# Kernel optimization log

Measured on AMD Instinct MI355X. Metric: run time of the kernel, lower is better.

The kernel has to match this reference:

```python
import jax, jax.numpy as jnp
import numpy as np

N_NODES = 100000
N_EDGES = 1600000
NEG_SLOPE = 0.2


def gat_layer(x, edge_index, W, att_src, att_dst, bias, concat):
    """PyG-style GATConv (v1) with self-loops added, dropout=0."""
    N = x.shape[0]
    H, C = att_src.shape
    ar = jnp.arange(N)
    src = jnp.concatenate([edge_index[0], ar])  # add self-loops
    dst = jnp.concatenate([edge_index[1], ar])
    h = (x @ W).reshape(N, H, C)                # [N,H,C]
    a_src = jnp.sum(h * att_src[None], axis=-1)  # [N,H]
    a_dst = jnp.sum(h * att_dst[None], axis=-1)  # [N,H]
    e = jax.nn.leaky_relu(a_src[src] + a_dst[dst], NEG_SLOPE)  # [E,H]
    # segment softmax over destination nodes
    m = jax.ops.segment_max(e, dst, num_segments=N)
    e = jnp.exp(e - m[dst])
    s = jax.ops.segment_sum(e, dst, num_segments=N)
    alpha = e / (s[dst] + 1e-16)                # [E,H]
    msg = h[src] * alpha[:, :, None]            # [E,H,C]
    out = jax.ops.segment_sum(msg, dst, num_segments=N)  # [N,H,C]
    if concat:
        out = out.reshape(N, H * C)
    else:
        out = out.mean(axis=1)
    return out + bias


def prelu(x, a):
    return jnp.where(x >= 0, x, a * x)


def setup_inputs() -> dict:
    key = jax.random.key(0)
    ks = jax.random.split(key, 12)
    def g(k, shape, fan):
        return jax.random.normal(k, shape, dtype=jnp.float32) * (1.0 / np.sqrt(fan))
    x = jax.random.normal(ks[0], (N_NODES, 256), dtype=jnp.float32)
    edge_index = jax.random.randint(ks[1], (2, N_EDGES), 0, N_NODES, dtype=jnp.int64 if jax.config.read('jax_enable_x64') else jnp.int32)
    return {
        'x': x,
        'edge_index': edge_index,
        'W1': g(ks[2], (256, 64), 256), 'as1': g(ks[3], (8, 8), 8), 'ad1': g(ks[4], (8, 8), 8), 'b1': jnp.zeros((64,), jnp.float32),
        'W2': g(ks[5], (320, 64), 320), 'as2': g(ks[6], (8, 8), 8), 'ad2': g(ks[7], (8, 8), 8), 'b2': jnp.zeros((64,), jnp.float32),
        'W3': g(ks[8], (64, 128), 64), 'as3': g(ks[9], (8, 16), 16), 'ad3': g(ks[10], (8, 16), 16), 'b3': jnp.zeros((16,), jnp.float32),
        'p1': jnp.full((1,), 0.25, jnp.float32), 'p2': jnp.full((1,), 0.25, jnp.float32),
    }


def reference(x, edge_index, W1, as1, ad1, b1, W2, as2, ad2, b2, W3, as3, ad3, b3, p1, p2):
    h = gat_layer(x, edge_index, W1, as1, ad1, b1, concat=True)
    h = prelu(h, p1)
    h = gat_layer(jnp.concatenate([x, h], axis=1), edge_index, W2, as2, ad2, b2, concat=True)
    h = prelu(h, p2)
    h = gat_layer(h, edge_index, W3, as3, ad3, b3, concat=False)
    return jax.nn.log_softmax(h, axis=1)
```

## Files before the change

kernel.cpp:

```cpp
#include <hip/hip_runtime.h>
#include <hip/hip_bf16.h>
#include <stdint.h>

typedef unsigned short u16;
typedef __attribute__((ext_vector_type(8))) short short8;
typedef __attribute__((ext_vector_type(8))) __bf16 bf16x8;
typedef __attribute__((ext_vector_type(4))) float f32x4;
typedef __attribute__((ext_vector_type(4))) float fv4;

#define DEV static __device__ __forceinline__

DEV float bf2f(u16 u) { uint32_t i = ((uint32_t)u) << 16; float f; __builtin_memcpy(&f, &i, 4); return f; }
DEV u16 f2bf(float f) {
    uint32_t i; __builtin_memcpy(&i, &f, 4);
    uint32_t r = i + 0x7FFFu + ((i >> 16) & 1u);
    return (u16)(r >> 16);
}
DEV float lo16f(uint32_t u) { uint32_t i = u << 16; float f; __builtin_memcpy(&f, &i, 4); return f; }
DEV float hi16f(uint32_t u) { uint32_t i = u & 0xFFFF0000u; float f; __builtin_memcpy(&f, &i, 4); return f; }
DEV uint32_t pack2(float a, float b) { return (uint32_t)f2bf(a) | ((uint32_t)f2bf(b) << 16); }
DEV float lrelu(float x) { return x >= 0.f ? x : 0.2f * x; }

#define CHK 4096
#define BN2SH 10
#define BN2 1024

__global__ __launch_bounds__(256) void k_cvt(const float* __restrict__ in, u16* __restrict__ out, int n4) {
    int i = blockIdx.x * 256 + threadIdx.x;
    if (i < n4) {
        fv4 v = __builtin_nontemporal_load((const fv4*)in + i);
        uint64_t o = (uint64_t)f2bf(v.x) | ((uint64_t)f2bf(v.y) << 16)
                   | ((uint64_t)f2bf(v.z) << 32) | ((uint64_t)f2bf(v.w) << 48);
        __builtin_nontemporal_store(o, (uint64_t*)out + i);
    }
}

__global__ __launch_bounds__(256) void k_hist(const int* __restrict__ dst, int* __restrict__ hist,
                                              int NBUK, int nbp, int E) {
    __shared__ int h[BN2];
    int tid = threadIdx.x;
    for (int i = tid; i < NBUK; i += 256) h[i] = 0;
    __syncthreads();
    int b0 = blockIdx.x * CHK;
    int jend = b0 + CHK < E ? b0 + CHK : E;
    for (int j = b0 + tid; j < jend; j += 256)
        atomicAdd(&h[dst[j] >> BN2SH], 1);
    __syncthreads();
    for (int i = tid; i < NBUK; i += 256) hist[i * nbp + blockIdx.x] = h[i];
}

__global__ void k_scanpart(const int* __restrict__ deg, int* __restrict__ bsum, int n) {
    __shared__ int buf[1024];
    int tid = threadIdx.x;
    int i = blockIdx.x * 1024 + tid;
    int v = (i < n) ? deg[i] : 0;
    buf[tid] = v; __syncthreads();
    for (int d = 512; d > 0; d >>= 1) {
        if (tid < d) buf[tid] += buf[tid + d];
        __syncthreads();
    }
    if (tid == 0) bsum[blockIdx.x] = buf[0];
}

__global__ void k_scanbsum(int* bsum, int nb) {
    if (threadIdx.x == 0) {
        int run = 0;
        for (int b = 0; b < nb; ++b) { int t = bsum[b]; bsum[b] = run; run += t; }
    }
}

__global__ void k_scanonly(const int* __restrict__ in, const int* __restrict__ bsum,
                           int* __restrict__ out, int n) {
    __shared__ int buf[1024];
    int tid = threadIdx.x;
    int i = blockIdx.x * 1024 + tid;
    int v = (i < n) ? in[i] : 0;
    buf[tid] = v; __syncthreads();
    for (int d = 1; d < 1024; d <<= 1) {
        int t = (tid >= d) ? buf[tid - d] : 0;
        __syncthreads();
        buf[tid] += t;
        __syncthreads();
    }
    if (i < n) out[i] = buf[tid] - v + bsum[blockIdx.x];
}

__global__ __launch_bounds__(256) void k_part(const int* __restrict__ src, const int* __restrict__ dst,
                                              const int* __restrict__ scanned, int* __restrict__ stage,
                                              int NBUK, int nbp, int E) {
    __shared__ int cur[BN2];
    int tid = threadIdx.x;
    for (int i = tid; i < NBUK; i += 256) cur[i] = scanned[i * nbp + blockIdx.x];
    __syncthreads();
    int b0 = blockIdx.x * CHK;
    int jend = b0 + CHK < E ? b0 + CHK : E;
    for (int j = b0 + tid; j < jend; j += 256) {
        int d = dst[j];
        int p = atomicAdd(&cur[d >> BN2SH], 1);
        stage[p] = src[j] | ((d & (BN2 - 1)) << 17);
    }
}

__global__ __launch_bounds__(256) void k_csr(const int* __restrict__ stage, const int* __restrict__ scanned,
                                             int* __restrict__ off, int* __restrict__ srt,
                                             int NBUK, int nbp, int N, int E) {
    __shared__ int deg[BN2];
    __shared__ int ex[BN2];
    __shared__ int tsum[256];
    int tid = threadIdx.x, b = blockIdx.x;
    int base = b << BN2SH;
    int s0 = scanned[b * nbp];
    int s1 = (b + 1 < NBUK) ? scanned[(b + 1) * nbp] : E;
    for (int i = tid; i < BN2; i += 256) deg[i] = 0;
    __syncthreads();
    for (int j = s0 + tid; j < s1; j += 256) atomicAdd(&deg[(uint32_t)stage[j] >> 17], 1);
    __syncthreads();
    int t4 = tid * 4;
    int d0 = deg[t4], d1 = deg[t4 + 1], d2 = deg[t4 + 2], d3 = deg[t4 + 3];
    int tot = d0 + d1 + d2 + d3;
    tsum[tid] = tot; __syncthreads();
    for (int d = 1; d < 256; d <<= 1) {
        int t = (tid >= d) ? tsum[tid - d] : 0;
        __syncthreads();
        tsum[tid] += t;
        __syncthreads();
    }
    int ebase = tsum[tid] - tot;
    ex[t4] = ebase; ex[t4 + 1] = ebase + d0; ex[t4 + 2] = ebase + d0 + d1; ex[t4 + 3] = ebase + d0 + d1 + d2;
    __syncthreads();
    for (int i = tid; i < BN2; i += 256) { int n = base + i; if (n < N) off[n] = s0 + ex[i]; }
    if (b == 0 && tid == 0) off[N] = E;
    __syncthreads();
    for (int j = s0 + tid; j < s1; j += 256) {
        int sd = stage[j];
        int p = atomicAdd(&ex[(uint32_t)sd >> 17], 1);
        srt[s0 + p] = sd & 0x1FFFF;
    }
}

__global__ __launch_bounds__(256) void gemm_k(const u16* __restrict__ A1, int K1,
                                              const u16* __restrict__ A2, int K2,
                                              const float* __restrict__ W, int M,
                                              u16* __restrict__ out, int N) {
    __shared__ u16 wt[64][328];
    __shared__ u16 As[64][40];
    const int K = K1 + K2;
    const int tid = threadIdx.x;
    const int n0 = blockIdx.x * 64;
    const int cb = blockIdx.y * 64;

    for (int idx = tid; idx < K * 64; idx += 256) {
        int k = idx >> 6, m = idx & 63;
        wt[m][k] = f2bf(W[(size_t)k * M + cb + m]);
    }

    const int wv = tid >> 6, lane = tid & 63;
    const int quad = lane >> 4, r = lane & 15;
    f32x4 acc[4];
#pragma unroll
    for (int ct = 0; ct < 4; ++ct) acc[ct] = (f32x4){0.f, 0.f, 0.f, 0.f};

    const int row = tid >> 2, seg = tid & 3;
    const int gl = n0 + row;

    for (int k0 = 0; k0 < K; k0 += 32) {
        int4 v = {0, 0, 0, 0};
        if (gl < N) {
            const u16* base = (k0 < K1) ? (A1 + (size_t)gl * K1 + k0)
                                        : (A2 + (size_t)gl * K2 + (k0 - K1));
            v = *(const int4*)(base + seg * 8);
        }
        *(int4*)&As[row][seg * 8] = v;
        __syncthreads();
        bf16x8 a = __builtin_bit_cast(bf16x8, *(const short8*)&As[wv * 16 + r][quad * 8]);
#pragma unroll
        for (int ct = 0; ct < 4; ++ct) {
            bf16x8 b = __builtin_bit_cast(bf16x8, *(const short8*)&wt[ct * 16 + r][k0 + quad * 8]);
            acc[ct] = __builtin_amdgcn_mfma_f32_16x16x32_bf16(a, b, acc[ct], 0, 0, 0);
        }
        __syncthreads();
    }

#pragma unroll
    for (int ct = 0; ct < 4; ++ct)
#pragma unroll
        for (int rg = 0; rg < 4; ++rg) {
            int grow = n0 + wv * 16 + quad * 4 + rg;
            if (grow < N) out[(size_t)grow * M + cb + ct * 16 + r] = f2bf(acc[ct][rg]);
        }
}

__global__ __launch_bounds__(256) void acomp8(const u16* __restrict__ g,
                                              const float* __restrict__ ats, const float* __restrict__ atd,
                                              float* __restrict__ a_src, float* __restrict__ a_dst, int N) {
    int lane = threadIdx.x & 63;
    int node = blockIdx.x * 4 + (threadIdx.x >> 6);
    if (node >= N) return;
    float val = bf2f(g[(size_t)node * 64 + lane]);
    float ps = val * ats[lane];
    float pd = val * atd[lane];
#pragma unroll
    for (int d = 1; d < 8; d <<= 1) { ps += __shfl_xor(ps, d); pd += __shfl_xor(pd, d); }
    if ((lane & 7) == 0) {
        a_src[node * 8 + (lane >> 3)] = ps;
        a_dst[node * 8 + (lane >> 3)] = pd;
    }
}

__global__ __launch_bounds__(256) void acomp16(const u16* __restrict__ g,
                                               const float* __restrict__ ats, const float* __restrict__ atd,
                                               float* __restrict__ a_src, float* __restrict__ a_dst, int N) {
    int lane = threadIdx.x & 63;
    int node = blockIdx.x * 4 + (threadIdx.x >> 6);
    if (node >= N) return;
    float v0 = bf2f(g[(size_t)node * 128 + lane]);
    float v1 = bf2f(g[(size_t)node * 128 + lane + 64]);
    float ps0 = v0 * ats[lane],      pd0 = v0 * atd[lane];
    float ps1 = v1 * ats[lane + 64], pd1 = v1 * atd[lane + 64];
#pragma unroll
    for (int d = 1; d < 16; d <<= 1) {
        ps0 += __shfl_xor(ps0, d); pd0 += __shfl_xor(pd0, d);
        ps1 += __shfl_xor(ps1, d); pd1 += __shfl_xor(pd1, d);
    }
    if ((lane & 15) == 0) {
        int hd = lane >> 4;
        a_src[node * 8 + hd] = ps0;     a_dst[node * 8 + hd] = pd0;
        a_src[node * 8 + hd + 4] = ps1; a_dst[node * 8 + hd + 4] = pd1;
    }
}

__global__ __launch_bounds__(256) void agg12(const u16* __restrict__ g,
                                             const float* __restrict__ a_src, const float* __restrict__ a_dst,
                                             const int* __restrict__ off, const int* __restrict__ srt,
                                             const float* __restrict__ bias, const float* __restrict__ pslope,
                                             u16* __restrict__ hout, int N) {
    int tid = threadIdx.x;
    int lane32 = tid & 31;
    int node = blockIdx.x * 8 + (tid >> 5);
    int nd = node < N ? node : N - 1;
    int hd = lane32 >> 2;
    int hw = lane32 & 7;
    int e4 = lane32 >> 3;
    float ad_acc = a_dst[nd * 8 + hd];
    float ad_w   = a_dst[nd * 8 + hw];
    float ws = __expf(lrelu(a_src[nd * 8 + hd] + ad_acc));
    uint32_t gs = *(const uint32_t*)(g + (size_t)nd * 64 + lane32 * 2);
    float s = ws;
    float acc0 = ws * lo16f(gs), acc1 = ws * hi16f(gs);
    int jb = off[nd], je = off[nd + 1];
    int addrH = (tid & 32) * 4;
    int addrW = addrH + hd * 4;
    int idx = 0; float asv = 0.f;
    if (jb < je) {
        int jc = jb + e4; jc = jc < je ? jc : je - 1;
        idx = srt[jc];
        asv = a_src[idx * 8 + hw];
    }
    for (int j = jb; j < je; j += 4) {
        int cnt = je - j;
        float w = __expf(lrelu(asv + ad_w));
        int wi = __builtin_bit_cast(int, w);
        int jn = j + 4 + e4; jn = jn < je ? jn : je - 1;
        int idx_n = srt[jn];
        float as_n = a_src[idx_n * 8 + hw];
#pragma unroll
        for (int t = 0; t < 4; ++t) {
            int srcv = __builtin_amdgcn_ds_bpermute(addrH + t * 32, idx);
            int wvi  = __builtin_amdgcn_ds_bpermute(addrW + t * 32, wi);
            float wv = (t < cnt) ? __builtin_bit_cast(float, wvi) : 0.f;
            uint32_t gv = *(const uint32_t*)(g + (size_t)srcv * 64 + lane32 * 2);
            s += wv;
            acc0 += wv * lo16f(gv);
            acc1 += wv * hi16f(gv);
        }
        idx = idx_n; asv = as_n;
    }
    float r = 1.f / (s + 1e-16f);
    float2 bv = *(const float2*)(bias + lane32 * 2);
    float p = pslope[0];
    float v0 = acc0 * r + bv.x; v0 = v0 >= 0.f ? v0 : p * v0;
    float v1 = acc1 * r + bv.y; v1 = v1 >= 0.f ? v1 : p * v1;
    if (node < N) *(uint32_t*)(hout + (size_t)node * 64 + lane32 * 2) = pack2(v0, v1);
}

__global__ __launch_bounds__(256) void agg3(const u16* __restrict__ g,
                                            const float* __restrict__ a_src, const float* __restrict__ a_dst,
                                            const int* __restrict__ off, const int* __restrict__ srt,
                                            const float* __restrict__ b3, float* __restrict__ out, int N) {
    int tid = threadIdx.x;
    int lane = tid & 63;
    int node = blockIdx.x * 4 + (tid >> 6);
    int nd = node < N ? node : N - 1;
    int hd = lane >> 3;
    int hw = lane & 7;
    float ad_acc = a_dst[nd * 8 + hd];
    float ad_w   = a_dst[nd * 8 + hw];
    float ws = __expf(lrelu(a_src[nd * 8 + hd] + ad_acc));
    uint32_t gs = *(const uint32_t*)(g + (size_t)nd * 128 + lane * 2);
    float s = ws;
    float acc0 = ws * lo16f(gs), acc1 = ws * hi16f(gs);
    int jb = off[nd], je = off[nd + 1];
    int addrW = hd * 4;
    int idx = 0; float asv = 0.f;
    if (jb < je) {
        int jc = jb + hd; jc = jc < je ? jc : je - 1;
        idx = srt[jc];
        asv = a_src[idx * 8 + hw];
    }
    for (int j = jb; j < je; j += 8) {
        int cnt = je - j;
        float w = __expf(lrelu(asv + ad_w));
        int wi = __builtin_bit_cast(int, w);
        int jn = j + 8 + hd; jn = jn < je ? jn : je - 1;
        int idx_n = srt[jn];
        float as_n = a_src[idx_n * 8 + hw];
#pragma unroll
        for (int t = 0; t < 8; ++t) {
            int srcv = __builtin_amdgcn_readlane(idx, t * 8);
            int wvi  = __builtin_amdgcn_ds_bpermute(addrW + t * 32, wi);
            float wv = (t < cnt) ? __builtin_bit_cast(float, wvi) : 0.f;
            uint32_t gv = *(const uint32_t*)(g + (size_t)srcv * 128 + lane * 2);
            s += wv;
            acc0 += wv * lo16f(gv);
            acc1 += wv * hi16f(gv);
        }
        idx = idx_n; asv = as_n;
    }
    float r = 1.f / (s + 1e-16f);
    float v0 = acc0 * r, v1 = acc1 * r;
    v0 += __shfl_xor(v0, 8);  v1 += __shfl_xor(v1, 8);
    v0 += __shfl_xor(v0, 16); v1 += __shfl_xor(v1, 16);
    v0 += __shfl_xor(v0, 32); v1 += __shfl_xor(v1, 32);
    int c0 = (lane & 7) * 2;
    float2 bv = *(const float2*)(b3 + c0);
    float mean0 = v0 * 0.125f + bv.x, mean1 = v1 * 0.125f + bv.y;
    float m = fmaxf(mean0, mean1);
    m = fmaxf(m, __shfl_xor(m, 1)); m = fmaxf(m, __shfl_xor(m, 2)); m = fmaxf(m, __shfl_xor(m, 4));
    float se = __expf(mean0 - m) + __expf(mean1 - m);
    se += __shfl_xor(se, 1); se += __shfl_xor(se, 2); se += __shfl_xor(se, 4);
    float lg = __logf(se);
    if (node < N && lane < 8) {
        float2 o; o.x = mean0 - m - lg; o.y = mean1 - m - lg;
        *(float2*)(out + (size_t)node * 16 + c0) = o;
    }
}

extern "C" void kernel_launch(void* const* d_in, const int* in_sizes, int n_in,
                              void* d_out, int out_size, void* d_ws, size_t ws_size,
                              hipStream_t stream) {
    (void)n_in; (void)out_size; (void)ws_size;
    const float* x  = (const float*)d_in[0];
    const int* ei   = (const int*)d_in[1];
    const float* W1 = (const float*)d_in[2];
    const float* as1 = (const float*)d_in[3];
    const float* ad1 = (const float*)d_in[4];
    const float* b1  = (const float*)d_in[5];
    const float* W2  = (const float*)d_in[6];
    const float* as2 = (const float*)d_in[7];
    const float* ad2 = (const float*)d_in[8];
    const float* b2  = (const float*)d_in[9];
    const float* W3  = (const float*)d_in[10];
    const float* as3 = (const float*)d_in[11];
    const float* ad3 = (const float*)d_in[12];
    const float* b3  = (const float*)d_in[13];
    const float* p1  = (const float*)d_in[14];
    const float* p2  = (const float*)d_in[15];
    const int N = in_sizes[0] / 256;
    const int E = in_sizes[1] / 2;
    const int NBUK = (N + BN2 - 1) >> BN2SH;
    const int nbp = (E + CHK - 1) / CHK;
    const int nsc = NBUK * nbp;

    char* ws = (char*)d_ws;
    size_t o = 0;
    auto alloc = [&](size_t bytes) { void* p = ws + o; o = (o + bytes + 255) & ~(size_t)255; return p; };
    int* off     = (int*)alloc((size_t)(N + 1) * 4);
    int* bsum    = (int*)alloc(4096);
    int* hist    = (int*)alloc((size_t)nsc * 4);
    int* scanned = (int*)alloc((size_t)nsc * 4);
    int* srt     = (int*)alloc((size_t)E * 4);
    int* stage   = (int*)alloc((size_t)E * 4);
    u16* xb      = (u16*)alloc((size_t)N * 256 * 2);
    u16* g       = (u16*)alloc((size_t)N * 128 * 2);
    float* a_src = (float*)alloc((size_t)N * 8 * 4);
    float* a_dst = (float*)alloc((size_t)N * 8 * 4);
    u16* h1      = (u16*)alloc((size_t)N * 64 * 2);
    u16* h2      = (u16*)alloc((size_t)N * 64 * 2);

    int n4 = N * 256 / 4;
    k_cvt<<<(n4 + 255) / 256, 256, 0, stream>>>(x, xb, n4);

    k_hist<<<nbp, 256, 0, stream>>>(ei + E, hist, NBUK, nbp, E);
    int nS = (nsc + 1023) / 1024;
    k_scanpart<<<nS, 1024, 0, stream>>>(hist, bsum, nsc);
    k_scanbsum<<<1, 64, 0, stream>>>(bsum, nS);
    k_scanonly<<<nS, 1024, 0, stream>>>(hist, bsum, scanned, nsc);
    k_part<<<nbp, 256, 0, stream>>>(ei, ei + E, scanned, stage, NBUK, nbp, E);
    k_csr<<<NBUK, 256, 0, stream>>>(stage, scanned, off, srt, NBUK, nbp, N, E);

    int nb64 = (N + 63) / 64;
    int nb4 = (N + 3) / 4;
    int nb8 = (N + 7) / 8;

    gemm_k<<<dim3(nb64, 1), 256, 0, stream>>>(xb, 256, (const u16*)nullptr, 0, W1, 64, g, N);
    acomp8<<<nb4, 256, 0, stream>>>(g, as1, ad1, a_src, a_dst, N);
    agg12<<<nb8, 256, 0, stream>>>(g, a_src, a_dst, off, srt, b1, p1, h1, N);

    gemm_k<<<dim3(nb64, 1), 256, 0, stream>>>(xb, 256, h1, 64, W2, 64, g, N);
    acomp8<<<nb4, 256, 0, stream>>>(g, as2, ad2, a_src, a_dst, N);
    agg12<<<nb8, 256, 0, stream>>>(g, a_src, a_dst, off, srt, b2, p2, h2, N);

    gemm_k<<<dim3(nb64, 2), 256, 0, stream>>>(h2, 64, (const u16*)nullptr, 0, W3, 128, g, N);
    acomp16<<<nb4, 256, 0, stream>>>(g, as3, ad3, a_src, a_dst, N);
    agg3<<<nb4, 256, 0, stream>>>(g, a_src, a_dst, off, srt, b3, (float*)d_out, N);
}
```

Before: 577.5 us.

## Fuse fp32-to-bf16 input conversion into first GEMM and widen aggregation gathers

```diff
diff --git a/kernel.cpp b/kernel.cpp
--- a/kernel.cpp
+++ b/kernel.cpp
@@ -24,16 +24,6 @@
 #define CHK 4096
 #define BN2SH 10
 #define BN2 1024
-
-__global__ __launch_bounds__(256) void k_cvt(const float* __restrict__ in, u16* __restrict__ out, int n4) {
-    int i = blockIdx.x * 256 + threadIdx.x;
-    if (i < n4) {
-        fv4 v = __builtin_nontemporal_load((const fv4*)in + i);
-        uint64_t o = (uint64_t)f2bf(v.x) | ((uint64_t)f2bf(v.y) << 16)
-                   | ((uint64_t)f2bf(v.z) << 32) | ((uint64_t)f2bf(v.w) << 48);
-        __builtin_nontemporal_store(o, (uint64_t*)out + i);
-    }
-}
 
 __global__ __launch_bounds__(256) void k_hist(const int* __restrict__ dst, int* __restrict__ hist,
                                               int NBUK, int nbp, int E) {
@@ -141,7 +131,9 @@
 __global__ __launch_bounds__(256) void gemm_k(const u16* __restrict__ A1, int K1,
                                               const u16* __restrict__ A2, int K2,
                                               const float* __restrict__ W, int M,
-                                              u16* __restrict__ out, int N) {
+                                              u16* __restrict__ out, int N,
+                                              const float* __restrict__ A1f,
+                                              u16* __restrict__ xbout) {
     __shared__ u16 wt[64][328];
     __shared__ u16 As[64][40];
     const int K = K1 + K2;
@@ -166,9 +158,18 @@
     for (int k0 = 0; k0 < K; k0 += 32) {
         int4 v = {0, 0, 0, 0};
         if (gl < N) {
-            const u16* base = (k0 < K1) ? (A1 + (size_t)gl * K1 + k0)
-                                        : (A2 + (size_t)gl * K2 + (k0 - K1));
-            v = *(const int4*)(base + seg * 8);
+            if (A1f) {
+                const float* fb = A1f + (size_t)gl * K + k0 + seg * 8;
+                fv4 f0 = *(const fv4*)fb;
+                fv4 f1 = *(const fv4*)(fb + 4);
+                v.x = (int)pack2(f0.x, f0.y); v.y = (int)pack2(f0.z, f0.w);
+                v.z = (int)pack2(f1.x, f1.y); v.w = (int)pack2(f1.z, f1.w);
+                if (cb == 0) *(int4*)(xbout + (size_t)gl * K + k0 + seg * 8) = v;
+            } else {
+                const u16* base = (k0 < K1) ? (A1 + (size_t)gl * K1 + k0)
+                                            : (A2 + (size_t)gl * K2 + (k0 - K1));
+                v = *(const int4*)(base + seg * 8);
+            }
         }
         *(int4*)&As[row][seg * 8] = v;
         __syncthreads();
@@ -238,18 +239,28 @@
     int lane32 = tid & 31;
     int node = blockIdx.x * 8 + (tid >> 5);
     int nd = node < N ? node : N - 1;
-    int hd = lane32 >> 2;
-    int hw = lane32 & 7;
-    int e4 = lane32 >> 3;
-    float ad_acc = a_dst[nd * 8 + hd];
+    int lane16 = lane32 & 15;
+    int sub    = lane32 >> 4;
+    int hg     = lane16 >> 1;
+    int hw     = lane32 & 7;
+    int e4     = lane32 >> 3;
+    const char* gb = (const char*)g;
+
+    float ad_acc = a_dst[nd * 8 + hg];
     float ad_w   = a_dst[nd * 8 + hw];
-    float ws = __expf(lrelu(a_src[nd * 8 + hd] + ad_acc));
-    uint32_t gs = *(const uint32_t*)(g + (size_t)nd * 64 + lane32 * 2);
-    float s = ws;
-    float acc0 = ws * lo16f(gs), acc1 = ws * hi16f(gs);
+    float ws = __expf(lrelu(a_src[nd * 8 + hg] + ad_acc));
+    float m0 = (sub == 0) ? ws : 0.f;
+    uint2 gs = *(const uint2*)(gb + ((size_t)nd << 7) + lane16 * 8);
+    float s = m0;
+    float acc0 = m0 * lo16f(gs.x), acc1 = m0 * hi16f(gs.x);
+    float acc2 = m0 * lo16f(gs.y), acc3 = m0 * hi16f(gs.y);
+
     int jb = off[nd], je = off[nd + 1];
     int addrH = (tid & 32) * 4;
-    int addrW = addrH + hd * 4;
+    int addrS = addrH + sub * 32;
+    int addrW = addrS + hg * 4;
+    int laneoff = lane16 * 8;
+
     int idx = 0; float asv = 0.f;
     if (jb < je) {
         int jc = jb + e4; jc = jc < je ? jc : je - 1;
@@ -257,30 +268,43 @@
         asv = a_src[idx * 8 + hw];
     }
     for (int j = jb; j < je; j += 4) {
-        int cnt = je - j;
         float w = __expf(lrelu(asv + ad_w));
+        w = (j + e4 < je) ? w : 0.f;
         int wi = __builtin_bit_cast(int, w);
         int jn = j + 4 + e4; jn = jn < je ? jn : je - 1;
         int idx_n = srt[jn];
         float as_n = a_src[idx_n * 8 + hw];
-#pragma unroll
-        for (int t = 0; t < 4; ++t) {
-            int srcv = __builtin_amdgcn_ds_bpermute(addrH + t * 32, idx);
-            int wvi  = __builtin_amdgcn_ds_bpermute(addrW + t * 32, wi);
-            float wv = (t < cnt) ? __builtin_bit_cast(float, wvi) : 0.f;
-            uint32_t gv = *(const uint32_t*)(g + (size_t)srcv * 64 + lane32 * 2);
-            s += wv;
-            acc0 += wv * lo16f(gv);
-            acc1 += wv * hi16f(gv);
-        }
+
+        int sv0 = __builtin_amdgcn_ds_bpermute(addrS,      idx);
+        int wb0 = __builtin_amdgcn_ds_bpermute(addrW,      wi);
+        int sv1 = __builtin_amdgcn_ds_bpermute(addrS + 64, idx);
+        int wb1 = __builtin_amdgcn_ds_bpermute(addrW + 64, wi);
+        uint2 g0 = *(const uint2*)(gb + (((uint32_t)sv0 << 7) + laneoff));
+        uint2 g1 = *(const uint2*)(gb + (((uint32_t)sv1 << 7) + laneoff));
+        float wv0 = __builtin_bit_cast(float, wb0);
+        float wv1 = __builtin_bit_cast(float, wb1);
+        s += wv0;
+        acc0 += wv0 * lo16f(g0.x); acc1 += wv0 * hi16f(g0.x);
+        acc2 += wv0 * lo16f(g0.y); acc3 += wv0 * hi16f(g0.y);
+        s += wv1;
+        acc0 += wv1 * lo16f(g1.x); acc1 += wv1 * hi16f(g1.x);
+        acc2 += wv1 * lo16f(g1.y); acc3 += wv1 * hi16f(g1.y);
         idx = idx_n; asv = as_n;
     }
-    float r = 1.f / (s + 1e-16f);
-    float2 bv = *(const float2*)(bias + lane32 * 2);
-    float p = pslope[0];
-    float v0 = acc0 * r + bv.x; v0 = v0 >= 0.f ? v0 : p * v0;
-    float v1 = acc1 * r + bv.y; v1 = v1 >= 0.f ? v1 : p * v1;
-    if (node < N) *(uint32_t*)(hout + (size_t)node * 64 + lane32 * 2) = pack2(v0, v1);
+    s    += __shfl_xor(s,    16);
+    acc0 += __shfl_xor(acc0, 16); acc1 += __shfl_xor(acc1, 16);
+    acc2 += __shfl_xor(acc2, 16); acc3 += __shfl_xor(acc3, 16);
+    if (node < N && sub == 0) {
+        float r = 1.f / (s + 1e-16f);
+        fv4 bv = *(const fv4*)(bias + lane16 * 4);
+        float p = pslope[0];
+        float v0 = acc0 * r + bv.x; v0 = v0 >= 0.f ? v0 : p * v0;
+        float v1 = acc1 * r + bv.y; v1 = v1 >= 0.f ? v1 : p * v1;
+        float v2 = acc2 * r + bv.z; v2 = v2 >= 0.f ? v2 : p * v2;
+        float v3 = acc3 * r + bv.w; v3 = v3 >= 0.f ? v3 : p * v3;
+        uint2 o; o.x = pack2(v0, v1); o.y = pack2(v2, v3);
+        *(uint2*)((char*)hout + ((size_t)node << 7) + lane16 * 8) = o;
+    }
 }
 
 __global__ __launch_bounds__(256) void agg3(const u16* __restrict__ g,
@@ -291,57 +315,76 @@
     int lane = tid & 63;
     int node = blockIdx.x * 4 + (tid >> 6);
     int nd = node < N ? node : N - 1;
-    int hd = lane >> 3;
+    int lane32 = lane & 31;
+    int sub = lane >> 5;
+    int hg = lane32 >> 2;
     int hw = lane & 7;
-    float ad_acc = a_dst[nd * 8 + hd];
+    int e8 = lane >> 3;
+    const char* gb = (const char*)g;
+
+    float ad_acc = a_dst[nd * 8 + hg];
     float ad_w   = a_dst[nd * 8 + hw];
-    float ws = __expf(lrelu(a_src[nd * 8 + hd] + ad_acc));
-    uint32_t gs = *(const uint32_t*)(g + (size_t)nd * 128 + lane * 2);
-    float s = ws;
-    float acc0 = ws * lo16f(gs), acc1 = ws * hi16f(gs);
+    float ws = __expf(lrelu(a_src[nd * 8 + hg] + ad_acc));
+    float m0 = (sub == 0) ? ws : 0.f;
+    uint2 gs = *(const uint2*)(gb + ((size_t)nd << 8) + lane32 * 8);
+    float s = m0;
+    float acc0 = m0 * lo16f(gs.x), acc1 = m0 * hi16f(gs.x);
+    float acc2 = m0 * lo16f(gs.y), acc3 = m0 * hi16f(gs.y);
+
     int jb = off[nd], je = off[nd + 1];
-    int addrW = hd * 4;
+    int addrS = sub * 32;
+    int addrW = addrS + hg * 4;
+    int laneoff = lane32 * 8;
+
     int idx = 0; float asv = 0.f;
     if (jb < je) {
-        int jc = jb + hd; jc = jc < je ? jc : je - 1;
+        int jc = jb + e8; jc = jc < je ? jc : je - 1;
         idx = srt[jc];
         asv = a_src[idx * 8 + hw];
     }
     for (int j = jb; j < je; j += 8) {
-        int cnt = je - j;
         float w = __expf(lrelu(asv + ad_w));
+        w = (j + e8 < je) ? w : 0.f;
         int wi = __builtin_bit_cast(int, w);
-        int jn = j + 8 + hd; jn = jn < je ? jn : je - 1;
+        int jn = j + 8 + e8; jn = jn < je ? jn : je - 1;
         int idx_n = srt[jn];
         float as_n = a_src[idx_n * 8 + hw];
 #pragma unroll
-        for (int t = 0; t < 8; ++t) {
-            int srcv = __builtin_amdgcn_readlane(idx, t * 8);
-            int wvi  = __builtin_amdgcn_ds_bpermute(addrW + t * 32, wi);
-            float wv = (t < cnt) ? __builtin_bit_cast(float, wvi) : 0.f;
-            uint32_t gv = *(const uint32_t*)(g + (size_t)srcv * 128 + lane * 2);
-            s += wv;
-            acc0 += wv * lo16f(gv);
-            acc1 += wv * hi16f(gv);
+        for (int t = 0; t < 4; ++t) {
+            int sv = __builtin_amdgcn_ds_bpermute(addrS + t * 64, idx);
+            int wb = __builtin_amdgcn_ds_bpermute(addrW + t * 64, wi);
+            uint2 gv = *(const uint2*)(gb + (((uint32_t)sv << 8) + laneoff));
+            float wf = __builtin_bit_cast(float, wb);
+            s += wf;
+            acc0 += wf * lo16f(gv.x); acc1 += wf * hi16f(gv.x);
+            acc2 += wf * lo16f(gv.y); acc3 += wf * hi16f(gv.y);
         }
         idx = idx_n; asv = as_n;
     }
+    s    += __shfl_xor(s,    32);
+    acc0 += __shfl_xor(acc0, 32); acc1 += __shfl_xor(acc1, 32);
+    acc2 += __shfl_xor(acc2, 32); acc3 += __shfl_xor(acc3, 32);
     float r = 1.f / (s + 1e-16f);
-    float v0 = acc0 * r, v1 = acc1 * r;
-    v0 += __shfl_xor(v0, 8);  v1 += __shfl_xor(v1, 8);
-    v0 += __shfl_xor(v0, 16); v1 += __shfl_xor(v1, 16);
-    v0 += __shfl_xor(v0, 32); v1 += __shfl_xor(v1, 32);
-    int c0 = (lane & 7) * 2;
-    float2 bv = *(const float2*)(b3 + c0);
-    float mean0 = v0 * 0.125f + bv.x, mean1 = v1 * 0.125f + bv.y;
-    float m = fmaxf(mean0, mean1);
-    m = fmaxf(m, __shfl_xor(m, 1)); m = fmaxf(m, __shfl_xor(m, 2)); m = fmaxf(m, __shfl_xor(m, 4));
-    float se = __expf(mean0 - m) + __expf(mean1 - m);
-    se += __shfl_xor(se, 1); se += __shfl_xor(se, 2); se += __shfl_xor(se, 4);
+    acc0 *= r; acc1 *= r; acc2 *= r; acc3 *= r;
+#pragma unroll
+    for (int d = 4; d <= 16; d <<= 1) {
+        acc0 += __shfl_xor(acc0, d); acc1 += __shfl_xor(acc1, d);
+        acc2 += __shfl_xor(acc2, d); acc3 += __shfl_xor(acc3, d);
+    }
+    fv4 bv = *(const fv4*)(b3 + (lane32 & 3) * 4);
+    float v0 = acc0 * 0.125f + bv.x;
+    float v1 = acc1 * 0.125f + bv.y;
+    float v2 = acc2 * 0.125f + bv.z;
+    float v3 = acc3 * 0.125f + bv.w;
+    float m = fmaxf(fmaxf(v0, v1), fmaxf(v2, v3));
+    m = fmaxf(m, __shfl_xor(m, 1)); m = fmaxf(m, __shfl_xor(m, 2));
+    float se = __expf(v0 - m) + __expf(v1 - m) + __expf(v2 - m) + __expf(v3 - m);
+    se += __shfl_xor(se, 1); se += __shfl_xor(se, 2);
     float lg = __logf(se);
-    if (node < N && lane < 8) {
-        float2 o; o.x = mean0 - m - lg; o.y = mean1 - m - lg;
-        *(float2*)(out + (size_t)node * 16 + c0) = o;
+    if (node < N && lane < 4) {
+        float4 o;
+        o.x = v0 - m - lg; o.y = v1 - m - lg; o.z = v2 - m - lg; o.w = v3 - m - lg;
+        *(float4*)(out + (size_t)node * 16 + lane * 4) = o;
     }
 }
 
@@ -387,9 +430,6 @@
     u16* h1      = (u16*)alloc((size_t)N * 64 * 2);
     u16* h2      = (u16*)alloc((size_t)N * 64 * 2);
 
-    int n4 = N * 256 / 4;
-    k_cvt<<<(n4 + 255) / 256, 256, 0, stream>>>(x, xb, n4);
-
     k_hist<<<nbp, 256, 0, stream>>>(ei + E, hist, NBUK, nbp, E);
     int nS = (nsc + 1023) / 1024;
     k_scanpart<<<nS, 1024, 0, stream>>>(hist, bsum, nsc);
@@ -402,15 +442,15 @@
     int nb4 = (N + 3) / 4;
     int nb8 = (N + 7) / 8;
 
-    gemm_k<<<dim3(nb64, 1), 256, 0, stream>>>(xb, 256, (const u16*)nullptr, 0, W1, 64, g, N);
+    gemm_k<<<dim3(nb64, 1), 256, 0, stream>>>(xb, 256, (const u16*)nullptr, 0, W1, 64, g, N, x, xb);
     acomp8<<<nb4, 256, 0, stream>>>(g, as1, ad1, a_src, a_dst, N);
     agg12<<<nb8, 256, 0, stream>>>(g, a_src, a_dst, off, srt, b1, p1, h1, N);
 
-    gemm_k<<<dim3(nb64, 1), 256, 0, stream>>>(xb, 256, h1, 64, W2, 64, g, N);
+    gemm_k<<<dim3(nb64, 1), 256, 0, stream>>>(xb, 256, h1, 64, W2, 64, g, N, nullptr, nullptr);
     acomp8<<<nb4, 256, 0, stream>>>(g, as2, ad2, a_src, a_dst, N);
     agg12<<<nb8, 256, 0, stream>>>(g, a_src, a_dst, off, srt, b2, p2, h2, N);
 
-    gemm_k<<<dim3(nb64, 2), 256, 0, stream>>>(h2, 64, (const u16*)nullptr, 0, W3, 128, g, N);
+    gemm_k<<<dim3(nb64, 2), 256, 0, stream>>>(h2, 64, (const u16*)nullptr, 0, W3, 128, g, N, nullptr, nullptr);
     acomp16<<<nb4, 256, 0, stream>>>(g, as3, ad3, a_src, a_dst, N);
     agg3<<<nb4, 256, 0, stream>>>(g, a_src, a_dst, off, srt, b3, (float*)d_out, N);
 }
```

Result: no change. 584.7 us (+1.2%).
